# Optimization experiments

Hardware: AMD Instinct MI355X
Metric: run time of the kernel (lower is better)

The kernel has to match this reference:

```python
import jax, jax.numpy as jnp
import numpy as np

N = 4096      # n_patches / nodes
IN_FEAT = 512
EMBED = 512
HEADS = 8
HEAD_DIM = EMBED // HEADS
SCALING = HEAD_DIM ** -0.5


def setup_inputs() -> dict:
    key = jax.random.key(0)
    ks = jax.random.split(key, 7)
    x = jax.random.normal(ks[0], (N, IN_FEAT), dtype=jnp.float32)
    adj = jax.random.randint(ks[1], (N, N), 0, 2, dtype=jnp.int32)
    s = 0.04  # ~xavier scale for 512x512
    WQ = jax.random.normal(ks[2], (EMBED, IN_FEAT), dtype=jnp.float32) * s
    WK = jax.random.normal(ks[3], (EMBED, IN_FEAT), dtype=jnp.float32) * s
    WV = jax.random.normal(ks[4], (EMBED, IN_FEAT), dtype=jnp.float32) * s
    we = jax.random.normal(ks[5], (1, HEAD_DIM), dtype=jnp.float32) * 0.1
    be = jnp.zeros((1,), dtype=jnp.float32)
    return {"x": x, "adj": adj, "WQ": WQ, "WK": WK, "WV": WV, "we": we, "be": be}


def reference(x, adj, WQ, WK, WV, we, be):
    n = x.shape[0]
    # projections: [N, E] -> [H, N, head_dim]
    Q = (x @ WQ.T).reshape(n, HEADS, HEAD_DIM).transpose(1, 0, 2)
    K = (x @ WK.T).reshape(n, HEADS, HEAD_DIM).transpose(1, 0, 2)
    V = (x @ WV.T).reshape(n, HEADS, HEAD_DIM).transpose(1, 0, 2)
    # scores + per-query energy term: [H, N, N]
    energy = Q @ we.T + be                      # [H, N, 1]
    attn = jnp.einsum('hqd,hkd->hqk', Q, K) * SCALING + energy
    # adjacency mask (broadcast over heads)
    attn = attn + jnp.where(adj > 0, 0.0, -jnp.inf)
    attn = jax.nn.softmax(attn, axis=-1)
    # winner-take-all: one-hot at row max, divided by num_heads
    hard = (attn == jnp.max(attn, axis=-1, keepdims=True)).astype(jnp.float32) / HEADS
    out = jnp.einsum('hqk,hkd->hqd', hard, V)   # [H, N, head_dim]
    return out.transpose(1, 0, 2).reshape(n, EMBED)
```

## Files before the change

kernel.cpp:

```cpp
#include <hip/hip_runtime.h>
#include <hip/hip_bf16.h>
#include <float.h>
#include <stdint.h>

#define NPT    4096
#define EMB    512
#define NH     8
#define HD     64
#define KSPLIT 32

typedef __attribute__((ext_vector_type(8))) _Float16 f16x8;
typedef __attribute__((ext_vector_type(4))) float f32x4;
typedef uint32_t u32;

#define LO_SCALE 2048.0f
#define LO_INV   4.8828125e-4f

__device__ __forceinline__ void async_ld16(const void* gsrc, void* ldst) {
    __builtin_amdgcn_global_load_lds(
        (const __attribute__((address_space(1))) u32*)gsrc,
        (__attribute__((address_space(3))) u32*)ldst, 16, 0, 0);
}

__device__ __forceinline__ void split2(float a, unsigned short& h, unsigned short& l) {
    _Float16 fh = (_Float16)a;
    float r = (a - (float)fh) * LO_SCALE;
    _Float16 fl = (_Float16)r;
    h = *reinterpret_cast<unsigned short*>(&fh);
    l = *reinterpret_cast<unsigned short*>(&fl);
}

__global__ __launch_bounds__(256) void prep_kernel(const float* __restrict__ x,
                                                   const float* __restrict__ wq,
                                                   const float* __restrict__ wk,
                                                   const float* __restrict__ wv,
                                                   const int* __restrict__ adj,
                                                   unsigned short* __restrict__ xs,
                                                   unsigned short* __restrict__ wqs,
                                                   unsigned short* __restrict__ wks,
                                                   unsigned short* __restrict__ wvs,
                                                   unsigned* __restrict__ bits_t) {
    int y = blockIdx.y;
    size_t i = (size_t)blockIdx.x * 256 + threadIdx.x;
    if (y == 4) {
        int q = (int)(i >> 7), w = (int)i & 127;
        const int4* p = (const int4*)(adj + (size_t)q * NPT + w * 32);
        unsigned m = 0;
#pragma unroll
        for (int j = 0; j < 8; ++j) {
            int4 v = p[j];
            m |= (v.x != 0 ? 1u : 0u) << (j * 4 + 0);
            m |= (v.y != 0 ? 1u : 0u) << (j * 4 + 1);
            m |= (v.z != 0 ? 1u : 0u) << (j * 4 + 2);
            m |= (v.w != 0 ? 1u : 0u) << (j * 4 + 3);
        }
        bits_t[(size_t)w * NPT + q] = m;
    } else if (y == 0) {
        const size_t PL = (size_t)NPT * EMB;
        float4 v = ((const float4*)x)[i];
        ushort4 h, l;
        split2(v.x, h.x, l.x);
        split2(v.y, h.y, l.y);
        split2(v.z, h.z, l.z);
        split2(v.w, h.w, l.w);
        ((ushort4*)xs)[i]        = h;
        ((ushort4*)(xs + PL))[i] = l;
    } else {
        const size_t WPL = 262144;
        if (i >= WPL / 4) return;
        const float* src = (y == 1) ? wq : (y == 2) ? wk : wv;
        unsigned short* dst = (y == 1) ? wqs : (y == 2) ? wks : wvs;
        float4 v = ((const float4*)src)[i];
        int e  = (int)(i >> 7);
        int k0 = ((int)i & 127) * 4;
        int ebk = e >> 6, el = e & 63;
        int kc = k0 >> 5, g = (k0 >> 3) & 3, dd = k0 & 7;
        size_t off = ((((size_t)ebk * 16 + kc) * 4 + g) * 64 + el) * 8 + dd;
        ushort4 h, l;
        split2(v.x, h.x, l.x);
        split2(v.y, h.y, l.y);
        split2(v.z, h.z, l.z);
        split2(v.w, h.w, l.w);
        *(ushort4*)(dst + off)       = h;
        *(ushort4*)(dst + WPL + off) = l;
    }
}

__global__ __launch_bounds__(256, 3) void gemm_mfma(const unsigned short* __restrict__ xs,
                                                    const unsigned short* __restrict__ wqs,
                                                    const unsigned short* __restrict__ wks,
                                                    const unsigned short* __restrict__ wvs,
                                                    unsigned short* __restrict__ Q2,
                                                    unsigned short* __restrict__ K2,
                                                    float* __restrict__ V) {
    const int z = blockIdx.z;
    const unsigned short* W2 = (z == 0) ? wqs : (z == 1) ? wks : wvs;
    const size_t XPL = (size_t)NPT * EMB;
    const size_t WPL = 262144;
    const size_t OPL = (size_t)NH * NPT * HD;

    const int nb = blockIdx.x * 128;
    const int ebk = blockIdx.y;
    const int tid = threadIdx.x;
    const int wv = tid >> 6, lane = tid & 63;
    const int m = lane & 15, quad = lane >> 4;
    const int n0 = nb + wv * 32;

    __shared__ __align__(16) unsigned short Ws[2][2 * 2048];

    auto prefetchW = [&](int kc, int buf) {
#pragma unroll
        for (int i2 = 0; i2 < 2; ++i2) {
            int c = wv + 4 * i2;
            int p = c >> 2, sub = c & 3;
            const unsigned short* src = W2 + (size_t)p * WPL
                + ((size_t)ebk * 16 + kc) * 2048 + (sub * 64 + lane) * 8;
            async_ld16(src, &Ws[buf][p * 2048 + sub * 512]);
        }
    };
    f16x8 bfA[2][2], bfB[2][2];
    auto load_bf = [&](f16x8 (&bf)[2][2], int kc) {
#pragma unroll
        for (int nt = 0; nt < 2; ++nt)
#pragma unroll
            for (int p = 0; p < 2; ++p)
                bf[nt][p] = *(const f16x8*)(xs + (size_t)p * XPL
                    + (size_t)(n0 + nt * 16 + m) * EMB + kc * 32 + quad * 8);
    };

    f32x4 acc[2][4][2];
#pragma unroll
    for (int s = 0; s < 2; ++s)
#pragma unroll
        for (int mt = 0; mt < 4; ++mt)
#pragma unroll
            for (int nt = 0; nt < 2; ++nt) acc[s][mt][nt] = (f32x4){0.f, 0.f, 0.f, 0.f};

    prefetchW(0, 0);
    load_bf(bfA, 0);

    auto iter = [&](int kc, int buf, f16x8 (&cur)[2][2], f16x8 (&nxt)[2][2]) {
        asm volatile("s_waitcnt vmcnt(4)\n\ts_barrier" ::: "memory");
        if (kc < 15) { prefetchW(kc + 1, buf ^ 1); load_bf(nxt, kc + 1); }
#pragma unroll
        for (int ga = 0; ga < 2; ++ga) {
            f16x8 af[4];
#pragma unroll
            for (int mt = 0; mt < 4; ++mt)
                af[mt] = *(const f16x8*)&Ws[buf][ga * 2048 + (quad * 64 + mt * 16 + m) * 8];
#pragma unroll
            for (int pb = 0; pb < 2 - ga; ++pb)
#pragma unroll
                for (int mt = 0; mt < 4; ++mt)
#pragma unroll
                    for (int nt = 0; nt < 2; ++nt)
                        acc[ga + pb][mt][nt] = __builtin_amdgcn_mfma_f32_16x16x32_f16(
                            af[mt], cur[nt][pb], acc[ga + pb][mt][nt], 0, 0, 0);
        }
    };

#pragma unroll 1
    for (int kc2 = 0; kc2 < 16; kc2 += 2) {
        iter(kc2, 0, bfA, bfB);
        iter(kc2 + 1, 1, bfB, bfA);
    }

    const int h = ebk;
#pragma unroll
    for (int mt = 0; mt < 4; ++mt)
#pragma unroll
        for (int nt = 0; nt < 2; ++nt) {
            const int n = n0 + nt * 16 + m;
            const int d0 = mt * 16 + quad * 4;
            f32x4 a;
#pragma unroll
            for (int j = 0; j < 4; ++j)
                a[j] = fmaf(acc[1][mt][nt][j], LO_INV, acc[0][mt][nt][j]);
            if (z == 2) {
                *(f32x4*)(V + (size_t)n * EMB + ebk * 64 + d0) = a;
            } else {
                ushort4 ph, pl;
                split2(a[0], ph.x, pl.x);
                split2(a[1], ph.y, pl.y);
                split2(a[2], ph.z, pl.z);
                split2(a[3], ph.w, pl.w);
                unsigned short* O2 = (z == 0) ? Q2 : K2;
                size_t off = ((size_t)h * 128 + (n >> 5)) * 2048
                           + (d0 >> 3) * 256 + (n & 31) * 8 + (d0 & 7);
                *(ushort4*)(O2 + off)       = ph;
                *(ushort4*)(O2 + OPL + off) = pl;
            }
        }
}

__global__ __launch_bounds__(256, 4) void score_mfma(const unsigned short* __restrict__ Q2,
                                                     const unsigned short* __restrict__ K2,
                                                     const unsigned* __restrict__ bits_t,
                                                     float* __restrict__ pval,
                                                     int* __restrict__ pidx) {
    const int qb = blockIdx.x * 128;
    const int ks = blockIdx.y;
    const int tid = threadIdx.x;
    const int wv = tid >> 6, lane = tid & 63;
    const int m = lane & 15, quad = lane >> 4;
    const size_t PL = (size_t)NH * NPT * HD;
    const int kq = qb + wv * 32;

    __shared__ __align__(16) unsigned short Ks[3][2 * 2048];

    auto prefetchK = [&](int t) {
        int h = t >> 2, kt = ks * 4 + (t & 3), buf = t % 3;
#pragma unroll
        for (int i2 = 0; i2 < 2; ++i2) {
            int c = wv + 4 * i2;
            int p = c >> 2, sub = c & 3;
            const unsigned short* src = K2 + (size_t)p * PL
                + ((size_t)h * 128 + kt) * 2048 + (sub * 64 + lane) * 8;
            async_ld16(src, &Ks[buf][p * 2048 + sub * 512]);
        }
    };

    f16x8 qf[2][2][2];
    auto load_qf = [&](int hh) {
#pragma unroll
        for (int nt = 0; nt < 2; ++nt)
#pragma unroll
            for (int dc = 0; dc < 2; ++dc)
#pragma unroll
                for (int p = 0; p < 2; ++p)
                    qf[nt][dc][p] = *(const f16x8*)(Q2 + (size_t)p * PL
                        + ((size_t)hh * 128 + (kq >> 5)) * 2048
                        + (dc * 4 + quad) * 256 + (nt * 16 + m) * 8);
    };

    load_qf(0);
    prefetchK(0);
    prefetchK(1);

    float bestv[2]; int besti[2];

#pragma unroll 1
    for (int t = 0; t < NH * 4; ++t) {
        const int h = t >> 2, kst = t & 3, buf = t % 3;
        const int kbase = ks * 128 + kst * 32;

        asm volatile("s_waitcnt vmcnt(2)\n\ts_barrier" ::: "memory");

        if (kst == 0) { bestv[0] = bestv[1] = -FLT_MAX; besti[0] = besti[1] = 0; }

        unsigned bw[2];
#pragma unroll
        for (int nt = 0; nt < 2; ++nt)
            bw[nt] = bits_t[(size_t)(ks * 4 + kst) * NPT + kq + nt * 16 + m];

        f32x4 acc[2][2][2];
#pragma unroll
        for (int s = 0; s < 2; ++s)
#pragma unroll
            for (int mt = 0; mt < 2; ++mt)
#pragma unroll
                for (int nt = 0; nt < 2; ++nt) acc[s][mt][nt] = (f32x4){0.f, 0.f, 0.f, 0.f};

#pragma unroll
        for (int ga = 0; ga < 2; ++ga) {
            f16x8 kf[2][2];
#pragma unroll
            for (int mt = 0; mt < 2; ++mt)
#pragma unroll
                for (int dc = 0; dc < 2; ++dc)
                    kf[mt][dc] = *(const f16x8*)
                        &Ks[buf][ga * 2048 + ((dc * 4 + quad) * 32 + mt * 16 + m) * 8];
#pragma unroll
            for (int pb = 0; pb < 2 - ga; ++pb)
#pragma unroll
                for (int dc = 0; dc < 2; ++dc)
#pragma unroll
                    for (int mt = 0; mt < 2; ++mt)
#pragma unroll
                        for (int nt = 0; nt < 2; ++nt)
                            acc[ga + pb][mt][nt] = __builtin_amdgcn_mfma_f32_16x16x32_f16(
                                kf[mt][dc], qf[nt][dc][pb], acc[ga + pb][mt][nt], 0, 0, 0);
        }

        if (kst == 3 && h + 1 < NH) load_qf(h + 1);
        if (t + 2 < NH * 4) prefetchK(t + 2);

#pragma unroll
        for (int nt = 0; nt < 2; ++nt) {
            unsigned w = bw[nt];
#pragma unroll
            for (int mt = 0; mt < 2; ++mt) {
                int k0 = mt * 16 + quad * 4;
                f32x4 a0 = acc[0][mt][nt], a1 = acc[1][mt][nt];
#pragma unroll
                for (int r = 0; r < 4; ++r) {
                    if ((w >> (k0 + r)) & 1u) {
                        float s = fmaf(a1[r], LO_INV, a0[r]);
                        if (s > bestv[nt]) { bestv[nt] = s; besti[nt] = kbase + k0 + r; }
                    }
                }
            }
        }

        if (kst == 3) {
#pragma unroll
            for (int nt = 0; nt < 2; ++nt) {
                float v = bestv[nt]; int bi = besti[nt];
#pragma unroll
                for (int off = 16; off < 64; off <<= 1) {
                    float ov = __shfl_xor(v, off);
                    int   oi = __shfl_xor(bi, off);
                    if (ov > v || (ov == v && oi < bi)) { v = ov; bi = oi; }
                }
                if (quad == 0) {
                    size_t o = ((size_t)h * KSPLIT + ks) * NPT + kq + nt * 16 + m;
                    pval[o] = v; pidx[o] = bi;
                }
            }
        }
    }
}

__global__ __launch_bounds__(128) void gather_out(const float* __restrict__ V,
                                                  const float* __restrict__ pval,
                                                  const int* __restrict__ pidx,
                                                  float* __restrict__ out) {
    const int q = blockIdx.x;
    const int tid = threadIdx.x;
    __shared__ int widx[NH];
    if (tid < NH) {
        float bv = -FLT_MAX; int bi = 0;
        for (int ks = 0; ks < KSPLIT; ++ks) {
            size_t off = ((size_t)tid * KSPLIT + ks) * NPT + q;
            float v = pval[off];
            if (v > bv) { bv = v; bi = pidx[off]; }
        }
        widx[tid] = bi;
    }
    __syncthreads();
    const int h = tid >> 4;
    const int d4 = (tid & 15) * 4;
    const int k = widx[h];
    float4 v = *(const float4*)(V + (size_t)k * EMB + h * HD + d4);
    v.x *= 0.125f; v.y *= 0.125f; v.z *= 0.125f; v.w *= 0.125f;
    *(float4*)(out + (size_t)q * EMB + h * HD + d4) = v;
}

extern "C" void kernel_launch(void* const* d_in, const int* in_sizes, int n_in,
                              void* d_out, int out_size, void* d_ws, size_t ws_size,
                              hipStream_t stream) {
    const float* x   = (const float*)d_in[0];
    const int*   adj = (const int*)d_in[1];
    const float* WQ  = (const float*)d_in[2];
    const float* WK  = (const float*)d_in[3];
    const float* WV  = (const float*)d_in[4];
    float* out = (float*)d_out;

    char* ws = (char*)d_ws;
    const size_t HMB = 512u * 1024;
    unsigned short* xs   = (unsigned short*)(ws);
    unsigned short* wqs  = (unsigned short*)(ws + 16 * HMB);
    unsigned short* wks  = (unsigned short*)(ws + 18 * HMB);
    unsigned short* wvs  = (unsigned short*)(ws + 20 * HMB);
    unsigned short* Q2   = (unsigned short*)(ws + 22 * HMB);
    unsigned short* K2   = (unsigned short*)(ws + 38 * HMB);
    float*          V    = (float*)(ws + 54 * HMB);
    unsigned*       bits = (unsigned*)(ws + 70 * HMB);
    float*          pval = (float*)(ws);
    int*            pidx = (int*)(ws + 8 * HMB);

    prep_kernel<<<dim3(2048, 5), dim3(256), 0, stream>>>(x, WQ, WK, WV, adj,
                                                         xs, wqs, wks, wvs, bits);
    gemm_mfma<<<dim3(NPT / 128, NH, 3), dim3(256), 0, stream>>>(xs, wqs, wks, wvs, Q2, K2, V);
    score_mfma<<<dim3(NPT / 128, KSPLIT), dim3(256), 0, stream>>>(Q2, K2, bits, pval, pidx);
    gather_out<<<dim3(NPT), dim3(128), 0, stream>>>(V, pval, pidx, out);
}
```

Baseline: 233.6 us.

## Load K fragments directly from global, branchless masked argmax, parallel gather reduction

```diff
diff --git a/kernel.cpp b/kernel.cpp
--- a/kernel.cpp
+++ b/kernel.cpp
@@ -206,20 +206,6 @@
     const size_t PL = (size_t)NH * NPT * HD;
     const int kq = qb + wv * 32;
 
-    __shared__ __align__(16) unsigned short Ks[3][2 * 2048];
-
-    auto prefetchK = [&](int t) {
-        int h = t >> 2, kt = ks * 4 + (t & 3), buf = t % 3;
-#pragma unroll
-        for (int i2 = 0; i2 < 2; ++i2) {
-            int c = wv + 4 * i2;
-            int p = c >> 2, sub = c & 3;
-            const unsigned short* src = K2 + (size_t)p * PL
-                + ((size_t)h * 128 + kt) * 2048 + (sub * 64 + lane) * 8;
-            async_ld16(src, &Ks[buf][p * 2048 + sub * 512]);
-        }
-    };
-
     f16x8 qf[2][2][2];
     auto load_qf = [&](int hh) {
 #pragma unroll
@@ -234,116 +220,120 @@
     };
 
     load_qf(0);
-    prefetchK(0);
-    prefetchK(1);
-
-    float bestv[2]; int besti[2];
 
 #pragma unroll 1
-    for (int t = 0; t < NH * 4; ++t) {
-        const int h = t >> 2, kst = t & 3, buf = t % 3;
-        const int kbase = ks * 128 + kst * 32;
-
-        asm volatile("s_waitcnt vmcnt(2)\n\ts_barrier" ::: "memory");
-
-        if (kst == 0) { bestv[0] = bestv[1] = -FLT_MAX; besti[0] = besti[1] = 0; }
-
-        unsigned bw[2];
-#pragma unroll
-        for (int nt = 0; nt < 2; ++nt)
-            bw[nt] = bits_t[(size_t)(ks * 4 + kst) * NPT + kq + nt * 16 + m];
-
-        f32x4 acc[2][2][2];
-#pragma unroll
-        for (int s = 0; s < 2; ++s)
-#pragma unroll
-            for (int mt = 0; mt < 2; ++mt)
-#pragma unroll
-                for (int nt = 0; nt < 2; ++nt) acc[s][mt][nt] = (f32x4){0.f, 0.f, 0.f, 0.f};
-
-#pragma unroll
-        for (int ga = 0; ga < 2; ++ga) {
-            f16x8 kf[2][2];
-#pragma unroll
-            for (int mt = 0; mt < 2; ++mt)
-#pragma unroll
-                for (int dc = 0; dc < 2; ++dc)
-                    kf[mt][dc] = *(const f16x8*)
-                        &Ks[buf][ga * 2048 + ((dc * 4 + quad) * 32 + mt * 16 + m) * 8];
-#pragma unroll
-            for (int pb = 0; pb < 2 - ga; ++pb)
-#pragma unroll
-                for (int dc = 0; dc < 2; ++dc)
-#pragma unroll
-                    for (int mt = 0; mt < 2; ++mt)
-#pragma unroll
-                        for (int nt = 0; nt < 2; ++nt)
-                            acc[ga + pb][mt][nt] = __builtin_amdgcn_mfma_f32_16x16x32_f16(
-                                kf[mt][dc], qf[nt][dc][pb], acc[ga + pb][mt][nt], 0, 0, 0);
-        }
-
-        if (kst == 3 && h + 1 < NH) load_qf(h + 1);
-        if (t + 2 < NH * 4) prefetchK(t + 2);
-
-#pragma unroll
-        for (int nt = 0; nt < 2; ++nt) {
-            unsigned w = bw[nt];
-#pragma unroll
-            for (int mt = 0; mt < 2; ++mt) {
-                int k0 = mt * 16 + quad * 4;
-                f32x4 a0 = acc[0][mt][nt], a1 = acc[1][mt][nt];
-#pragma unroll
-                for (int r = 0; r < 4; ++r) {
-                    if ((w >> (k0 + r)) & 1u) {
+    for (int h = 0; h < NH; ++h) {
+        float bestv[2]; int besti[2];
+        bestv[0] = bestv[1] = -FLT_MAX;
+        besti[0] = besti[1] = 0;
+
+#pragma unroll
+        for (int kst = 0; kst < 4; ++kst) {
+            const int kbase = ks * 128 + kst * 32;
+            const unsigned short* kb = K2 + ((size_t)h * 128 + ks * 4 + kst) * 2048;
+
+            unsigned bw[2];
+#pragma unroll
+            for (int nt = 0; nt < 2; ++nt)
+                bw[nt] = bits_t[(size_t)(ks * 4 + kst) * NPT + kq + nt * 16 + m];
+
+            f32x4 acc[2][2][2];
+#pragma unroll
+            for (int s = 0; s < 2; ++s)
+#pragma unroll
+                for (int mt = 0; mt < 2; ++mt)
+#pragma unroll
+                    for (int nt = 0; nt < 2; ++nt) acc[s][mt][nt] = (f32x4){0.f, 0.f, 0.f, 0.f};
+
+#pragma unroll
+            for (int ga = 0; ga < 2; ++ga) {
+                f16x8 kf[2][2];
+#pragma unroll
+                for (int mt = 0; mt < 2; ++mt)
+#pragma unroll
+                    for (int dc = 0; dc < 2; ++dc)
+                        kf[mt][dc] = *(const f16x8*)(kb + (size_t)ga * PL
+                            + (dc * 4 + quad) * 256 + (mt * 16 + m) * 8);
+#pragma unroll
+                for (int pb = 0; pb < 2 - ga; ++pb)
+#pragma unroll
+                    for (int dc = 0; dc < 2; ++dc)
+#pragma unroll
+                        for (int mt = 0; mt < 2; ++mt)
+#pragma unroll
+                            for (int nt = 0; nt < 2; ++nt)
+                                acc[ga + pb][mt][nt] = __builtin_amdgcn_mfma_f32_16x16x32_f16(
+                                    kf[mt][dc], qf[nt][dc][pb], acc[ga + pb][mt][nt], 0, 0, 0);
+            }
+
+            const int idxb = kbase + quad * 4;
+#pragma unroll
+            for (int nt = 0; nt < 2; ++nt) {
+                unsigned wq = bw[nt] >> (quad * 4);
+#pragma unroll
+                for (int mt = 0; mt < 2; ++mt) {
+                    f32x4 a0 = acc[0][mt][nt], a1 = acc[1][mt][nt];
+#pragma unroll
+                    for (int r = 0; r < 4; ++r) {
                         float s = fmaf(a1[r], LO_INV, a0[r]);
-                        if (s > bestv[nt]) { bestv[nt] = s; besti[nt] = kbase + k0 + r; }
+                        bool ok = (wq >> (mt * 16 + r)) & 1u;
+                        s = ok ? s : -FLT_MAX;
+                        int idx = idxb + mt * 16 + r;
+                        bool g = s > bestv[nt];
+                        bestv[nt] = g ? s : bestv[nt];
+                        besti[nt] = g ? idx : besti[nt];
                     }
                 }
             }
         }
 
-        if (kst == 3) {
-#pragma unroll
-            for (int nt = 0; nt < 2; ++nt) {
-                float v = bestv[nt]; int bi = besti[nt];
-#pragma unroll
-                for (int off = 16; off < 64; off <<= 1) {
-                    float ov = __shfl_xor(v, off);
-                    int   oi = __shfl_xor(bi, off);
-                    if (ov > v || (ov == v && oi < bi)) { v = ov; bi = oi; }
-                }
-                if (quad == 0) {
-                    size_t o = ((size_t)h * KSPLIT + ks) * NPT + kq + nt * 16 + m;
-                    pval[o] = v; pidx[o] = bi;
-                }
-            }
-        }
-    }
-}
-
-__global__ __launch_bounds__(128) void gather_out(const float* __restrict__ V,
+        if (h + 1 < NH) load_qf(h + 1);
+
+#pragma unroll
+        for (int nt = 0; nt < 2; ++nt) {
+            float v = bestv[nt]; int bi = besti[nt];
+#pragma unroll
+            for (int off = 16; off < 64; off <<= 1) {
+                float ov = __shfl_xor(v, off);
+                int   oi = __shfl_xor(bi, off);
+                if (ov > v || (ov == v && oi < bi)) { v = ov; bi = oi; }
+            }
+            if (quad == 0) {
+                size_t o = ((size_t)h * KSPLIT + ks) * NPT + kq + nt * 16 + m;
+                pval[o] = v; pidx[o] = bi;
+            }
+        }
+    }
+}
+
+__global__ __launch_bounds__(256) void gather_out(const float* __restrict__ V,
                                                   const float* __restrict__ pval,
                                                   const int* __restrict__ pidx,
                                                   float* __restrict__ out) {
     const int q = blockIdx.x;
     const int tid = threadIdx.x;
     __shared__ int widx[NH];
-    if (tid < NH) {
-        float bv = -FLT_MAX; int bi = 0;
-        for (int ks = 0; ks < KSPLIT; ++ks) {
-            size_t off = ((size_t)tid * KSPLIT + ks) * NPT + q;
-            float v = pval[off];
-            if (v > bv) { bv = v; bi = pidx[off]; }
-        }
-        widx[tid] = bi;
+    {
+        const int h = tid >> 5, ksl = tid & 31;
+        size_t off = ((size_t)h * KSPLIT + ksl) * NPT + q;
+        float v = pval[off]; int bi = pidx[off];
+#pragma unroll
+        for (int o = 1; o < 32; o <<= 1) {
+            float ov = __shfl_xor(v, o);
+            int   oi = __shfl_xor(bi, o);
+            if (ov > v || (ov == v && oi < bi)) { v = ov; bi = oi; }
+        }
+        if (ksl == 0) widx[h] = bi;
     }
     __syncthreads();
-    const int h = tid >> 4;
-    const int d4 = (tid & 15) * 4;
-    const int k = widx[h];
-    float4 v = *(const float4*)(V + (size_t)k * EMB + h * HD + d4);
-    v.x *= 0.125f; v.y *= 0.125f; v.z *= 0.125f; v.w *= 0.125f;
-    *(float4*)(out + (size_t)q * EMB + h * HD + d4) = v;
+    if (tid < 128) {
+        const int h = tid >> 4;
+        const int d4 = (tid & 15) * 4;
+        const int k = widx[h];
+        float4 v = *(const float4*)(V + (size_t)k * EMB + h * HD + d4);
+        v.x *= 0.125f; v.y *= 0.125f; v.z *= 0.125f; v.w *= 0.125f;
+        *(float4*)(out + (size_t)q * EMB + h * HD + d4) = v;
+    }
 }
 
 extern "C" void kernel_launch(void* const* d_in, const int* in_sizes, int n_in,
@@ -373,5 +363,5 @@
                                                          xs, wqs, wks, wvs, bits);
     gemm_mfma<<<dim3(NPT / 128, NH, 3), dim3(256), 0, stream>>>(xs, wqs, wks, wvs, Q2, K2, V);
     score_mfma<<<dim3(NPT / 128, KSPLIT), dim3(256), 0, stream>>>(Q2, K2, bits, pval, pidx);
-    gather_out<<<dim3(NPT), dim3(128), 0, stream>>>(V, pval, pidx, out);
-}
+    gather_out<<<dim3(NPT), dim3(256), 0, stream>>>(V, pval, pidx, out);
+}
```

New measurement: 421.5 us. +80.4%, slower.
